# Optimization experiments

Measured on AMD Instinct MI355X. Metric: run time of the kernel, lower is better.

## Reference

```python
import jax, jax.numpy as jnp
import numpy as np
from jax import lax


def setup_inputs() -> dict:
    key = jax.random.key(0)
    k1, k2, k3 = jax.random.split(key, 3)
    B, Ci, Co, K, H, W = 8, 512, 512, 3, 32, 32
    x = jax.random.normal(k1, (B, Ci, H, W), dtype=jnp.float32)
    y_s = jax.random.normal(k2, (B, Ci), dtype=jnp.float32)
    weight = jax.random.normal(k3, (Co, Ci, K, K), dtype=jnp.float32)  # scale_init = 1 (equal_lr)
    bias = jnp.zeros((Co,), dtype=jnp.float32)
    return {"x": x, "y_s": y_s, "weight": weight, "bias": bias}


def reference(x, y_s, weight, bias):
    # equal_lr=True -> runtime scale = (in_channels * k^2) ** -0.5
    Co, Ci, K, _ = weight.shape
    scale_forward = (Ci * K * K) ** -0.5
    w = scale_forward * weight  # [Co, Ci, K, K]

    # Fused StyleGAN2 trick (mathematically identical to per-sample grouped conv):
    # conv(x, y_s[b,i]*w[o,i]) == conv(x * y_s, w); demod divides by per-(b,o) norm.
    x_mod = x * y_s[:, :, None, None]
    out = lax.conv_general_dilated(
        x_mod, w,
        window_strides=(1, 1),
        padding=((1, 1), (1, 1)),
        rhs_dilation=(1, 1),
        dimension_numbers=("NCHW", "OIHW", "NCHW"),
    )  # [B, Co, H, W]

    # demod=True: x_s[b,o] = sqrt(sum_{i,kh,kw} (y_s[b,i]*w[o,i,kh,kw])^2 + 1e-8)
    w2 = jnp.sum(w * w, axis=(2, 3))  # [Co, Ci]
    xs = jnp.sqrt(jnp.einsum("bi,oi->bo", y_s * y_s, w2) + 1e-8)  # [B, Co]
    out = out / xs[:, :, None, None] + bias[None, :, None, None]
    return out
```

## Files before the change

### kernel.cpp

```cpp
#include <hip/hip_runtime.h>

typedef __attribute__((ext_vector_type(8))) short short8;
typedef __attribute__((ext_vector_type(4))) float f32x4;

#define RCP_OFF   0
#define WPRE_OFF  16384
#define XM_OFF    4734976

__device__ __forceinline__ unsigned short f2bf(float f) {
  unsigned int u = __float_as_uint(f);
  u += 0x7FFFu + ((u >> 16) & 1u);
  return (unsigned short)(u >> 16);
}

__device__ __forceinline__ void gload_lds16(const void* g, void* l) {
  __builtin_amdgcn_global_load_lds(
      (__attribute__((address_space(1))) void*)g,
      (__attribute__((address_space(3))) void*)l, 16, 0, 0);
}

__global__ __launch_bounds__(256) void prep_kernel(
    const float* __restrict__ x, const float* __restrict__ ys,
    const float* __restrict__ w,
    unsigned short* __restrict__ xm, unsigned short* __restrict__ wpre,
    float* __restrict__ rcp) {
  int bid = blockIdx.x;
  int tid = threadIdx.x;

  if (bid < 512) {
    int half = bid & 1;
    int h = (bid >> 1) & 31;
    int b = bid >> 6;
    __shared__ float tile[256][33];
    int ci0 = half * 256;
#pragma unroll
    for (int r = 0; r < 32; ++r) {
      int ci = r * 8 + (tid >> 5);
      int wcol = tid & 31;
      float v = x[(((size_t)b * 512 + ci0 + ci) * 32 + h) * 32 + wcol];
      tile[ci][wcol] = v * ys[b * 512 + ci0 + ci];
    }
    __syncthreads();
    int g0 = half * 32;
    for (int r = 0; r < 5; ++r) {
      int idx = r * 256 + tid;
      if (idx < 1088) {
        int gl = idx / 34;
        int col = idx - gl * 34;
        short8 v = {0,0,0,0,0,0,0,0};
        if (col != 0 && col != 33) {
          int wcol = col - 1;
#pragma unroll
          for (int j = 0; j < 8; ++j)
            v[j] = (short)f2bf(tile[gl * 8 + j][wcol]);
        }
        size_t off = ((((size_t)b * 64 + g0 + gl) * 34 + (h + 1)) * 34 + col) * 8;
        *reinterpret_cast<short8*>(xm + off) = v;
      }
    }
    if (h == 0 || h == 31) {
      int hp = (h == 0) ? 0 : 33;
      for (int r = 0; r < 5; ++r) {
        int idx = r * 256 + tid;
        if (idx < 1088) {
          int gl = idx / 34;
          int col = idx - gl * 34;
          short8 z = {0,0,0,0,0,0,0,0};
          size_t off = ((((size_t)b * 64 + g0 + gl) * 34 + hp) * 34 + col) * 8;
          *reinterpret_cast<short8*>(xm + off) = z;
        }
      }
    }
  } else if (bid < 640) {
    int pid = bid - 512;
    int coh = pid & 1;
    int kb = (pid >> 1) & 7;
    int c = pid >> 4;
    int co = coh * 256 + tid;
    int ci0 = c * 64 + kb * 8;
    const float* wp = w + (size_t)co * 4608 + (size_t)ci0 * 9;
    float v[72];
    const f32x4* wp4 = reinterpret_cast<const f32x4*>(wp);
#pragma unroll
    for (int i = 0; i < 18; ++i) {
      f32x4 q = wp4[i];
      v[i * 4 + 0] = q[0]; v[i * 4 + 1] = q[1]; v[i * 4 + 2] = q[2]; v[i * 4 + 3] = q[3];
    }
    const float scale = 1.4731391274719738e-02f;
#pragma unroll
    for (int t = 0; t < 9; ++t) {
      short8 s;
#pragma unroll
      for (int j = 0; j < 8; ++j) s[j] = (short)f2bf(scale * v[j * 9 + t]);
      *reinterpret_cast<short8*>(wpre + ((((size_t)c * 9 + t) * 8 + kb) * 512 + co) * 8) = s;
    }
  } else {
    int pid = bid - 640;
    int wv = tid >> 6;
    int lane = tid & 63;
    int o = pid * 4 + wv;
    const float* wp = w + (size_t)o * 4608 + (size_t)lane * 72;
    const float scale2 = 1.0f / 4608.0f;
    float w2[8];
#pragma unroll
    for (int j = 0; j < 8; ++j) {
      float s = 0.f;
#pragma unroll
      for (int k = 0; k < 9; ++k) { float vv = wp[j * 9 + k]; s += vv * vv; }
      w2[j] = s * scale2;
    }
#pragma unroll
    for (int b = 0; b < 8; ++b) {
      float p = 0.f;
#pragma unroll
      for (int j = 0; j < 8; ++j) {
        float y = ys[b * 512 + lane * 8 + j];
        p += y * y * w2[j];
      }
#pragma unroll
      for (int off = 32; off > 0; off >>= 1) p += __shfl_down(p, off);
      if (lane == 0) rcp[b * 512 + o] = 1.0f / sqrtf(p + 1e-8f);
    }
  }
}

__global__ __launch_bounds__(512, 1) void conv_main(
    const unsigned short* __restrict__ wpre,
    const unsigned short* __restrict__ xm,
    const float* __restrict__ rcp,
    const float* __restrict__ bias,
    float* __restrict__ out)
{
  __shared__ __align__(16) char smem[52224];

  int bid = blockIdx.x;
  int xcd = bid & 7;
  int j0 = bid >> 3;
  int cog = xcd >> 1;
  int sp = (xcd & 1) * 32 + j0;
  int b = sp >> 3;
  int hg = sp & 7;
  int tid = threadIdx.x;
  int lane = tid & 63;
  int wv = tid >> 6;
  int wc = wv & 1;
  int wr = (wv >> 1) & 1;
  int kp = wv >> 2;
  int l15 = lane & 15, l4 = lane >> 4;

  f32x4 acc[4][4];
#pragma unroll
  for (int i = 0; i < 4; ++i)
#pragma unroll
    for (int jj = 0; jj < 4; ++jj) { f32x4 z = {0.f,0.f,0.f,0.f}; acc[i][jj] = z; }

  const unsigned short* xmb = xm + (size_t)b * (64 * 34 * 34 * 8);
  const unsigned short* wbase =
      wpre + ((size_t)(kp * 4 + l4) * 512 + cog * 128 + wr * 64 + l15) * 8;

  auto stageX = [&](int c, int buf) {
    char* xb = smem + buf * 26112;
#pragma unroll
    for (int r = 0; r < 4; ++r) {
      int idx = r * 512 + tid;
      if (idx < 1632) {
        int kb = idx / 204;
        int rem = idx - kb * 204;
        int rr = rem / 34;
        int col = rem - rr * 34;
        const unsigned short* src =
            xmb + (((size_t)(c * 8 + kb) * 34 + hg * 4 + rr) * 34 + col) * 8;
        gload_lds16(src, xb + idx * 16);
      }
    }
  };

  auto loadA = [&](int ct, short8 (&a)[4]) {
    const unsigned short* p = wbase + (size_t)ct * 32768;
#pragma unroll
    for (int mi = 0; mi < 4; ++mi)
      a[mi] = *reinterpret_cast<const short8*>(p + mi * 128);
  };

  short8 X[4], Y[4], Z[4];

  stageX(0, 0);
  loadA(0, X);
  loadA(1, Y);
  __syncthreads();

  for (int c = 0; c < 8; ++c) {
    const char* xb = smem + (c & 1) * 26112;
    if (c < 7) stageX(c + 1, (c + 1) & 1);
#pragma unroll
    for (int t = 0; t < 9; ++t) {
      int ct = c * 9 + t;
      short8 (&cur)[4] = (t % 3 == 0) ? X : ((t % 3 == 1) ? Y : Z);
      short8 (&nxt)[4] = (t % 3 == 0) ? Z : ((t % 3 == 1) ? X : Y);
      if (ct < 70) loadA(ct + 2, nxt);
      int kh = t / 3, kw = t % 3;
#pragma unroll
      for (int nj = 0; nj < 4; ++nj) {
        int row4 = wc * 2 + (nj >> 1);
        int bo = (kp * 4 + l4) * 3264 + (row4 + kh) * 544 + ((nj & 1) * 16 + l15 + kw) * 16;
        short8 bfrag = *reinterpret_cast<const short8*>(xb + bo);
#pragma unroll
        for (int mi = 0; mi < 4; ++mi)
          acc[mi][nj] = __builtin_amdgcn_mfma_f32_16x16x32_bf16(cur[mi], bfrag, acc[mi][nj], 0, 0, 0);
      }
    }
    if (c < 7) {
      asm volatile("s_waitcnt vmcnt(8)" ::: "memory");
      __builtin_amdgcn_s_barrier();
      asm volatile("" ::: "memory");
    }
  }
  __syncthreads();

#pragma unroll
  for (int p = 0; p < 2; ++p) {
    if (kp == 1 && wr == p) {
#pragma unroll
      for (int mi = 0; mi < 4; ++mi)
#pragma unroll
        for (int nj = 0; nj < 4; ++nj)
          *reinterpret_cast<f32x4*>(smem + wc * 16384 + (mi * 4 + nj) * 1024 + lane * 16) = acc[mi][nj];
    }
    __syncthreads();
    if (kp == 0 && wr == p) {
#pragma unroll
      for (int mi = 0; mi < 4; ++mi)
#pragma unroll
        for (int nj = 0; nj < 4; ++nj) {
          f32x4 v = *reinterpret_cast<const f32x4*>(smem + wc * 16384 + (mi * 4 + nj) * 1024 + lane * 16);
          acc[mi][nj] = acc[mi][nj] + v;
        }
    }
    __syncthreads();
  }

  if (kp == 0) {
    const float* rcpb = rcp + b * 512;
#pragma unroll
    for (int mi = 0; mi < 4; ++mi) {
      int ob = cog * 128 + wr * 64 + mi * 16 + l4 * 4;
      float rc[4], bi[4];
#pragma unroll
      for (int jj = 0; jj < 4; ++jj) { rc[jj] = rcpb[ob + jj]; bi[jj] = bias[ob + jj]; }
#pragma unroll
      for (int nj = 0; nj < 4; ++nj) {
        int row4 = wc * 2 + (nj >> 1);
        int wcol = (nj & 1) * 16 + l15;
        int h = hg * 4 + row4;
#pragma unroll
        for (int jj = 0; jj < 4; ++jj)
          out[(((size_t)b * 512 + ob + jj) * 32 + h) * 32 + wcol] = acc[mi][nj][jj] * rc[jj] + bi[jj];
      }
    }
  }
}

extern "C" void kernel_launch(void* const* d_in, const int* in_sizes, int n_in,
                              void* d_out, int out_size, void* d_ws, size_t ws_size,
                              hipStream_t stream) {
  const float* x    = (const float*)d_in[0];
  const float* ys   = (const float*)d_in[1];
  const float* w    = (const float*)d_in[2];
  const float* bias = (const float*)d_in[3];
  float* out = (float*)d_out;
  char* ws = (char*)d_ws;
  float* rcp = (float*)(ws + RCP_OFF);
  unsigned short* wpre = (unsigned short*)(ws + WPRE_OFF);
  unsigned short* xm   = (unsigned short*)(ws + XM_OFF);

  prep_kernel<<<768, 256, 0, stream>>>(x, ys, w, xm, wpre, rcp);
  conv_main<<<256, 512, 0, stream>>>(wpre, xm, rcp, bias, out);
}
```

Before: 58.49 us.

## Retile conv into smaller 2-wave blocks without split-K reduction

The conv kernel moves from 256 blocks of 8 waves (with a split-K pair reduced through LDS) to 1024 blocks of 2 waves, each covering 64 output channels by 2 rows. Each wave now handles the full K for its tile, which removes the LDS cross-wave reduction and the extra barriers. B fragments are double-buffered in registers and A is loaded one step ahead, and the launch bound allows two blocks per CU. The intent is better occupancy and load balancing across the GPU, at the cost of less weight reuse per block and more redundant X staging.

```diff
diff --git a/kernel.cpp b/kernel.cpp
--- a/kernel.cpp
+++ b/kernel.cpp
@@ -124,138 +124,132 @@
   }
 }
 
-__global__ __launch_bounds__(512, 1) void conv_main(
+__global__ __launch_bounds__(128, 2) void conv_main(
     const unsigned short* __restrict__ wpre,
     const unsigned short* __restrict__ xm,
     const float* __restrict__ rcp,
     const float* __restrict__ bias,
     float* __restrict__ out)
 {
-  __shared__ __align__(16) char smem[52224];
+  __shared__ __align__(16) char smem[34816];
 
   int bid = blockIdx.x;
-  int xcd = bid & 7;
-  int j0 = bid >> 3;
-  int cog = xcd >> 1;
-  int sp = (xcd & 1) * 32 + j0;
-  int b = sp >> 3;
-  int hg = sp & 7;
+  int cog = bid & 7;
+  int sp = bid >> 3;
+  int b = sp >> 4;
+  int hp = sp & 15;
   int tid = threadIdx.x;
   int lane = tid & 63;
-  int wv = tid >> 6;
-  int wc = wv & 1;
-  int wr = (wv >> 1) & 1;
-  int kp = wv >> 2;
+  int wc = tid >> 6;
   int l15 = lane & 15, l4 = lane >> 4;
 
-  f32x4 acc[4][4];
+  f32x4 acc[4][2];
 #pragma unroll
   for (int i = 0; i < 4; ++i)
 #pragma unroll
-    for (int jj = 0; jj < 4; ++jj) { f32x4 z = {0.f,0.f,0.f,0.f}; acc[i][jj] = z; }
+    for (int jj = 0; jj < 2; ++jj) { f32x4 z = {0.f,0.f,0.f,0.f}; acc[i][jj] = z; }
 
   const unsigned short* xmb = xm + (size_t)b * (64 * 34 * 34 * 8);
-  const unsigned short* wbase =
-      wpre + ((size_t)(kp * 4 + l4) * 512 + cog * 128 + wr * 64 + l15) * 8;
+  const unsigned short* wbase = wpre + ((size_t)l4 * 512 + cog * 64 + l15) * 8;
+  const int bbase = (l4 * 4 + wc) * 544 + l15 * 16;
 
   auto stageX = [&](int c, int buf) {
-    char* xb = smem + buf * 26112;
-#pragma unroll
-    for (int r = 0; r < 4; ++r) {
-      int idx = r * 512 + tid;
-      if (idx < 1632) {
-        int kb = idx / 204;
-        int rem = idx - kb * 204;
-        int rr = rem / 34;
-        int col = rem - rr * 34;
-        const unsigned short* src =
-            xmb + (((size_t)(c * 8 + kb) * 34 + hg * 4 + rr) * 34 + col) * 8;
-        gload_lds16(src, xb + idx * 16);
-      }
-    }
-  };
-
-  auto loadA = [&](int ct, short8 (&a)[4]) {
+    char* xb = smem + buf * 17408;
+#pragma unroll
+    for (int i = 0; i < 8; ++i) {
+      int idx = i * 128 + tid;
+      int kbr = idx / 34;
+      int col = idx - kbr * 34;
+      const unsigned short* src =
+          xmb + (((size_t)(c * 8 + (kbr >> 2)) * 34 + 2 * hp + (kbr & 3)) * 34 + col) * 8;
+      gload_lds16(src, xb + idx * 16);
+    }
+    if (tid < 64) {
+      int idx = 1024 + tid;
+      int kbr = idx / 34;
+      int col = idx - kbr * 34;
+      const unsigned short* src =
+          xmb + (((size_t)(c * 8 + (kbr >> 2)) * 34 + 2 * hp + (kbr & 3)) * 34 + col) * 8;
+      gload_lds16(src, xb + idx * 16);
+    }
+  };
+
+  auto loadA = [&](int ct, short8 (&a)[2][4]) {
     const unsigned short* p = wbase + (size_t)ct * 32768;
 #pragma unroll
-    for (int mi = 0; mi < 4; ++mi)
-      a[mi] = *reinterpret_cast<const short8*>(p + mi * 128);
-  };
-
-  short8 X[4], Y[4], Z[4];
-
-  stageX(0, 0);
-  loadA(0, X);
-  loadA(1, Y);
-  __syncthreads();
-
-  for (int c = 0; c < 8; ++c) {
-    const char* xb = smem + (c & 1) * 26112;
+    for (int ks = 0; ks < 2; ++ks)
+#pragma unroll
+      for (int mi = 0; mi < 4; ++mi)
+        a[ks][mi] = *reinterpret_cast<const short8*>(p + ks * 16384 + mi * 128);
+  };
+
+  auto loadB = [&](const char* xb, int t, short8 (&f)[2][2]) {
+    int kh = t / 3, kw = t % 3;
+#pragma unroll
+    for (int ks = 0; ks < 2; ++ks)
+#pragma unroll
+      for (int nj = 0; nj < 2; ++nj)
+        f[ks][nj] = *reinterpret_cast<const short8*>(
+            xb + bbase + ks * 8704 + kh * 544 + nj * 256 + kw * 16);
+  };
+
+  short8 A0[2][4], A1[2][4];
+
+  auto chunk = [&](int c, short8 (&Ae)[2][4], short8 (&Ao)[2][4]) {
+    const char* xb = smem + (c & 1) * 17408;
     if (c < 7) stageX(c + 1, (c + 1) & 1);
+    short8 Bp[2][2], Bq[2][2];
+    loadB(xb, 0, Bp);
 #pragma unroll
     for (int t = 0; t < 9; ++t) {
       int ct = c * 9 + t;
-      short8 (&cur)[4] = (t % 3 == 0) ? X : ((t % 3 == 1) ? Y : Z);
-      short8 (&nxt)[4] = (t % 3 == 0) ? Z : ((t % 3 == 1) ? X : Y);
-      if (ct < 70) loadA(ct + 2, nxt);
-      int kh = t / 3, kw = t % 3;
-#pragma unroll
-      for (int nj = 0; nj < 4; ++nj) {
-        int row4 = wc * 2 + (nj >> 1);
-        int bo = (kp * 4 + l4) * 3264 + (row4 + kh) * 544 + ((nj & 1) * 16 + l15 + kw) * 16;
-        short8 bfrag = *reinterpret_cast<const short8*>(xb + bo);
-#pragma unroll
-        for (int mi = 0; mi < 4; ++mi)
-          acc[mi][nj] = __builtin_amdgcn_mfma_f32_16x16x32_bf16(cur[mi], bfrag, acc[mi][nj], 0, 0, 0);
-      }
+      short8 (&curA)[2][4] = (t & 1) ? Ao : Ae;
+      short8 (&nxtA)[2][4] = (t & 1) ? Ae : Ao;
+      short8 (&curB)[2][2] = (t & 1) ? Bq : Bp;
+      short8 (&nxtB)[2][2] = (t & 1) ? Bp : Bq;
+      if (ct < 71) loadA(ct + 1, nxtA);
+      if (t < 8) loadB(xb, t + 1, nxtB);
+#pragma unroll
+      for (int ks = 0; ks < 2; ++ks)
+#pragma unroll
+        for (int nj = 0; nj < 2; ++nj)
+#pragma unroll
+          for (int mi = 0; mi < 4; ++mi)
+            acc[mi][nj] = __builtin_amdgcn_mfma_f32_16x16x32_bf16(
+                curA[ks][mi], curB[ks][nj], acc[mi][nj], 0, 0, 0);
     }
     if (c < 7) {
-      asm volatile("s_waitcnt vmcnt(8)" ::: "memory");
+      asm volatile("s_waitcnt vmcnt(8) lgkmcnt(0)" ::: "memory");
       __builtin_amdgcn_s_barrier();
       asm volatile("" ::: "memory");
     }
+  };
+
+  stageX(0, 0);
+  loadA(0, A0);
+  asm volatile("s_waitcnt vmcnt(8)" ::: "memory");
+  __builtin_amdgcn_s_barrier();
+  asm volatile("" ::: "memory");
+
+  for (int cc = 0; cc < 8; cc += 2) {
+    chunk(cc, A0, A1);
+    chunk(cc + 1, A1, A0);
   }
-  __syncthreads();
-
-#pragma unroll
-  for (int p = 0; p < 2; ++p) {
-    if (kp == 1 && wr == p) {
-#pragma unroll
-      for (int mi = 0; mi < 4; ++mi)
-#pragma unroll
-        for (int nj = 0; nj < 4; ++nj)
-          *reinterpret_cast<f32x4*>(smem + wc * 16384 + (mi * 4 + nj) * 1024 + lane * 16) = acc[mi][nj];
-    }
-    __syncthreads();
-    if (kp == 0 && wr == p) {
-#pragma unroll
-      for (int mi = 0; mi < 4; ++mi)
-#pragma unroll
-        for (int nj = 0; nj < 4; ++nj) {
-          f32x4 v = *reinterpret_cast<const f32x4*>(smem + wc * 16384 + (mi * 4 + nj) * 1024 + lane * 16);
-          acc[mi][nj] = acc[mi][nj] + v;
-        }
-    }
-    __syncthreads();
-  }
-
-  if (kp == 0) {
-    const float* rcpb = rcp + b * 512;
-#pragma unroll
-    for (int mi = 0; mi < 4; ++mi) {
-      int ob = cog * 128 + wr * 64 + mi * 16 + l4 * 4;
-      float rc[4], bi[4];
-#pragma unroll
-      for (int jj = 0; jj < 4; ++jj) { rc[jj] = rcpb[ob + jj]; bi[jj] = bias[ob + jj]; }
-#pragma unroll
-      for (int nj = 0; nj < 4; ++nj) {
-        int row4 = wc * 2 + (nj >> 1);
-        int wcol = (nj & 1) * 16 + l15;
-        int h = hg * 4 + row4;
-#pragma unroll
-        for (int jj = 0; jj < 4; ++jj)
-          out[(((size_t)b * 512 + ob + jj) * 32 + h) * 32 + wcol] = acc[mi][nj][jj] * rc[jj] + bi[jj];
-      }
+
+  const float* rcpb = rcp + b * 512;
+  int h = 2 * hp + wc;
+#pragma unroll
+  for (int mi = 0; mi < 4; ++mi) {
+    int ob = cog * 64 + mi * 16 + l4 * 4;
+    float rc[4], bi[4];
+#pragma unroll
+    for (int jj = 0; jj < 4; ++jj) { rc[jj] = rcpb[ob + jj]; bi[jj] = bias[ob + jj]; }
+#pragma unroll
+    for (int nj = 0; nj < 2; ++nj) {
+      int wcol = nj * 16 + l15;
+#pragma unroll
+      for (int jj = 0; jj < 4; ++jj)
+        out[(((size_t)b * 512 + ob + jj) * 32 + h) * 32 + wcol] = acc[mi][nj][jj] * rc[jj] + bi[jj];
     }
   }
 }
@@ -274,5 +268,5 @@
   unsigned short* xm   = (unsigned short*)(ws + XM_OFF);
 
   prep_kernel<<<768, 256, 0, stream>>>(x, ys, w, xm, wpre, rcp);
-  conv_main<<<256, 512, 0, stream>>>(wpre, xm, rcp, bias, out);
-}
+  conv_main<<<1024, 128, 0, stream>>>(wpre, xm, rcp, bias, out);
+}
```

Result: slower. 79.35 us (+35.7%).
